# Performance work log

Hardware: AMD Instinct MI355X
Metric: run time of the kernel (lower is better)

## Reference

```python
import jax, jax.numpy as jnp
import numpy as np

N, L, D, H = 2, 2048, 1024, 16
Dh = D // H          # 64
HIST = 2048          # history_len
SCALE = D ** 0.5     # note: module scales by sqrt(model_dim), not sqrt(head_dim)


def setup_inputs() -> dict:
    key = jax.random.key(0)
    ks = jax.random.split(key, 10)
    f = lambda k, s, sc=1.0: jax.random.normal(k, s, dtype=jnp.float32) * sc
    i = jnp.arange(L)
    causal = i[None, :] > i[:, None]            # mask future
    old = i[None, :] <= i[:, None] - HIST       # mask beyond history window
    mask = causal | old                          # True = masked, (L, L)
    return {
        "values": f(ks[0], (N, L, D)),
        "keys": f(ks[1], (N, L, D)),
        "query": f(ks[2], (N, L, D)),
        "origin_values": f(ks[3], (N, L, D)),
        "origin_keys": f(ks[4], (N, L, D)),
        "Wv": f(ks[5], (Dh, Dh), 0.1),
        "Wk": f(ks[6], (Dh, Dh), 0.1),
        "Wq": f(ks[7], (Dh, Dh), 0.1),
        "fc_w": f(ks[8], (D, D), 0.03),
        "fc_b": jnp.zeros((D,), dtype=jnp.float32),
        "mask": mask,
    }


def reference(values, keys, query, origin_values, origin_keys, Wv, Wk, Wq, fc_w, fc_b, mask):
    # forward(..., ref_sample=True): mfpca_attention path.
    # origin_keys/values are projected exactly as the prior ref_sample=False call stored them.
    split = lambda x: x.reshape(N, L, H, Dh)
    v = split(values) @ Wv.T        # (N, L, H, Dh)  torch Linear: x @ W^T, no bias
    k = split(keys) @ Wk.T
    q = split(query) @ Wq.T
    ov = split(origin_values) @ Wv.T
    ok = split(origin_keys) @ Wk.T

    energy = jnp.einsum('nqhd,nkhd->nhqk', q, ok)       # (N, H, L, L)
    samp_energy = jnp.einsum('nlhd,nlhd->nhl', q, k)    # (N, H, L)
    eye = jnp.eye(L, dtype=bool)
    # energy.diagonal().copy_(samp_energy)
    energy = jnp.where(eye, samp_energy[:, :, None, :], energy)
    energy = jnp.where(mask, jnp.float32(-1e20), energy)
    scores = jax.nn.softmax(energy / SCALE, axis=-1)
    diag_scores = jnp.diagonal(scores, axis1=2, axis2=3)    # (N, H, L)
    scores_nodiag = jnp.where(eye, 0.0, scores)
    # NOTE: original einsum output is indexed by l (not q) -- reproduced faithfully.
    origin_attention = jnp.einsum('nhql,nlhd->nlhd', scores_nodiag, ov)
    samp_attention = jnp.einsum('nhl,nlhd->nlhd', diag_scores, v)
    attention = (samp_attention + origin_attention).reshape(N, L, D)
    return attention @ fc_w.T + fc_b
```

## Files before the change

### kernel.cpp

```cpp
#include <hip/hip_runtime.h>

#define NB 2
#define LL 2048
#define DD 1024
#define HH 16
#define NHH (NB*HH)
#define LT (LL/64)
#define KT16 (LL/16)
#define CEXP 0.0450842200277801f

typedef __bf16 bf16x8 __attribute__((ext_vector_type(8)));
typedef unsigned short u16x8 __attribute__((ext_vector_type(8)));
typedef float f32x4 __attribute__((ext_vector_type(4)));

#define MFMA16 __builtin_amdgcn_mfma_f32_16x16x32_bf16
#define EXP2 __builtin_amdgcn_exp2f

__device__ __forceinline__ unsigned short f2bf(float f) {
    unsigned u = __float_as_uint(f);
    return (unsigned short)((u + 0x7fffu + ((u >> 16) & 1u)) >> 16);
}
__device__ __forceinline__ float bf2f(unsigned short u) {
    return __uint_as_float(((unsigned)u) << 16);
}
__device__ __forceinline__ bf16x8 ldfrag(const unsigned short* p) {
    return *reinterpret_cast<const bf16x8*>(p);
}
__device__ __forceinline__ bf16x8 cvt8v(float4 a, float4 b) {
    u16x8 u;
    u[0]=f2bf(a.x); u[1]=f2bf(a.y); u[2]=f2bf(a.z); u[3]=f2bf(a.w);
    u[4]=f2bf(b.x); u[5]=f2bf(b.y); u[6]=f2bf(b.z); u[7]=f2bf(b.w);
    return __builtin_bit_cast(bf16x8, u);
}
__device__ __forceinline__ ushort4 pack4(f32x4 d, float sc) {
    ushort4 o;
    o.x = f2bf(d[0]*sc); o.y = f2bf(d[1]*sc); o.z = f2bf(d[2]*sc); o.w = f2bf(d[3]*sc);
    return o;
}
__device__ __forceinline__ void gload16(const unsigned short* g, unsigned short* l) {
    __builtin_amdgcn_global_load_lds(
        (const __attribute__((address_space(1))) unsigned int*)g,
        (__attribute__((address_space(3))) unsigned int*)l, 16, 0, 0);
}

__global__ __launch_bounds__(256) void prep_kernel(
    const float* __restrict__ Wk, const float* __restrict__ Wq,
    const float* __restrict__ Wv, unsigned short* __restrict__ wfrag,
    const float* __restrict__ fc_w, unsigned short* __restrict__ fcwb)
{
    const int bid = blockIdx.x;
    const int t = threadIdx.x;
    if (bid < 6) {
        const int s = bid * 256 + t;
        const int m = s >> 9;
        const int rem = s & 511;
        const int f = rem >> 6;
        const int lane = rem & 63;
        const int n16 = lane & 15, quad = lane >> 4;
        const int mt = f >> 1, half = f & 1;
        const float* W = (m == 0) ? Wk : (m == 1) ? Wq : Wv;
        const float* p = W + (mt*16 + n16)*64 + quad*8 + half*32;
        float4 a = *reinterpret_cast<const float4*>(p);
        float4 b = *reinterpret_cast<const float4*>(p + 4);
        *reinterpret_cast<bf16x8*>(wfrag + (size_t)s * 8) = cvt8v(a, b);
    } else {
        const int idx = (bid - 6) * 1024 + t * 4;
        float4 wv = *reinterpret_cast<const float4*>(fc_w + idx);
        ushort4 o;
        o.x = f2bf(wv.x); o.y = f2bf(wv.y); o.z = f2bf(wv.z); o.w = f2bf(wv.w);
        *reinterpret_cast<ushort4*>(fcwb + idx) = o;
    }
}

__global__ __launch_bounds__(256) void proj_kernel(
    const float* __restrict__ values, const float* __restrict__ keys,
    const float* __restrict__ query,  const float* __restrict__ ovals,
    const float* __restrict__ okeys,  const unsigned short* __restrict__ wfrag,
    unsigned short* __restrict__ qb, unsigned short* __restrict__ okb,
    unsigned short* __restrict__ vb, unsigned short* __restrict__ ovb,
    float* __restrict__ ediag)
{
    const int t = threadIdx.x;
    const int w = t >> 6;
    const int lane = t & 63;
    const int n16 = lane & 15;
    const int quad = lane >> 4;
    const int h = blockIdx.y;
    const int row = blockIdx.x * 64 + w * 16 + n16;
    const int nn = row >> 11;
    const int ll = row & 2047;
    const size_t xoff  = (size_t)row * DD + h * 64 + quad * 8;
    const size_t qbase = (((size_t)(nn * HH + h)) * LL + ll) * 64;
    const size_t vbase = (size_t)row * DD + h * 64;

    if (blockIdx.z == 0) {
        const float4* kp = reinterpret_cast<const float4*>(keys  + xoff);
        const float4* qp = reinterpret_cast<const float4*>(query + xoff);
        const float4* op = reinterpret_cast<const float4*>(okeys + xoff);
        float4 k0 = kp[0], k1 = kp[1], k2 = kp[8], k3 = kp[9];
        float4 q0 = qp[0], q1 = qp[1], q2 = qp[8], q3 = qp[9];
        float4 o0 = op[0], o1 = op[1], o2 = op[8], o3 = op[9];
        bf16x8 wk[8], wq[8];
#pragma unroll
        for (int f = 0; f < 8; ++f) {
            wk[f] = ldfrag(wfrag + (size_t)(f * 64 + lane) * 8);
            wq[f] = ldfrag(wfrag + (size_t)((8 + f) * 64 + lane) * 8);
        }
        bf16x8 xk0 = cvt8v(k0, k1), xk1 = cvt8v(k2, k3);
        bf16x8 xq0 = cvt8v(q0, q1), xq1 = cvt8v(q2, q3);
        bf16x8 xo0 = cvt8v(o0, o1), xo1 = cvt8v(o2, o3);
        f32x4 ka[4], qa[4];
#pragma unroll
        for (int mt = 0; mt < 4; ++mt) {
            f32x4 d = {0.f,0.f,0.f,0.f};
            d = MFMA16(wk[mt*2], xk0, d, 0,0,0);
            ka[mt] = MFMA16(wk[mt*2+1], xk1, d, 0,0,0);
        }
#pragma unroll
        for (int mt = 0; mt < 4; ++mt) {
            f32x4 d = {0.f,0.f,0.f,0.f};
            d = MFMA16(wq[mt*2], xq0, d, 0,0,0);
            qa[mt] = MFMA16(wq[mt*2+1], xq1, d, 0,0,0);
            *reinterpret_cast<ushort4*>(qb + qbase + mt*16 + quad*4) = pack4(qa[mt], CEXP);
        }
#pragma unroll
        for (int mt = 0; mt < 4; ++mt) {
            f32x4 d = {0.f,0.f,0.f,0.f};
            d = MFMA16(wk[mt*2], xo0, d, 0,0,0);
            d = MFMA16(wk[mt*2+1], xo1, d, 0,0,0);
            *reinterpret_cast<ushort4*>(okb + qbase + mt*16 + quad*4) = pack4(d, 1.0f);
        }
        float p = 0.f;
#pragma unroll
        for (int mt = 0; mt < 4; ++mt)
            p += qa[mt][0]*ka[mt][0] + qa[mt][1]*ka[mt][1]
               + qa[mt][2]*ka[mt][2] + qa[mt][3]*ka[mt][3];
        p += __shfl_xor(p, 16);
        p += __shfl_xor(p, 32);
        if (lane < 16)
            ediag[((size_t)(nn * HH + h)) * LL + ll] = p;
    } else {
        const float4* vp = reinterpret_cast<const float4*>(values + xoff);
        const float4* op = reinterpret_cast<const float4*>(ovals  + xoff);
        float4 v0 = vp[0], v1 = vp[1], v2 = vp[8], v3 = vp[9];
        float4 o0 = op[0], o1 = op[1], o2 = op[8], o3 = op[9];
        bf16x8 wv[8];
#pragma unroll
        for (int f = 0; f < 8; ++f)
            wv[f] = ldfrag(wfrag + (size_t)((16 + f) * 64 + lane) * 8);
        bf16x8 xv0 = cvt8v(v0, v1), xv1 = cvt8v(v2, v3);
        bf16x8 xo0 = cvt8v(o0, o1), xo1 = cvt8v(o2, o3);
#pragma unroll
        for (int mt = 0; mt < 4; ++mt) {
            f32x4 d = {0.f,0.f,0.f,0.f};
            d = MFMA16(wv[mt*2], xv0, d, 0,0,0);
            d = MFMA16(wv[mt*2+1], xv1, d, 0,0,0);
            *reinterpret_cast<ushort4*>(vb + vbase + mt*16 + quad*4) = pack4(d, 1.0f);
        }
#pragma unroll
        for (int mt = 0; mt < 4; ++mt) {
            f32x4 d = {0.f,0.f,0.f,0.f};
            d = MFMA16(wv[mt*2], xo0, d, 0,0,0);
            d = MFMA16(wv[mt*2+1], xo1, d, 0,0,0);
            *reinterpret_cast<ushort4*>(ovb + vbase + mt*16 + quad*4) = pack4(d, 1.0f);
        }
    }
}

__global__ __launch_bounds__(256) void zrow_part(
    const unsigned short* __restrict__ qb, const unsigned short* __restrict__ okb,
    float* __restrict__ Zbuf)
{
    __shared__ unsigned short slds[2][64 * 64];

    const int bid = blockIdx.x;
    const int nh = bid & 31;
    const int qt = 31 - (bid >> 5);
    const int t = threadIdx.x;
    const int w = t >> 6;
    const int lane = t & 63;
    const int n = lane & 15;
    const int quad = lane >> 4;
    const size_t base = (size_t)nh * (LL * 64);
    const size_t nhL = (size_t)nh * LL;

    const unsigned short* bp = qb + base + (size_t)(qt*64 + w*16 + n) * 64 + quad * 8;
    const bf16x8 bq0 = ldfrag(bp);
    const bf16x8 bq1 = ldfrag(bp + 32);

    const int srow = t >> 3;
    const int schunk = (t & 7) ^ (srow & 7);
    const int soff = srow * 64 + schunk * 8;
    const int nst = qt + 1;

    {
        const unsigned short* s0 = okb + base + soff;
        gload16(s0, &slds[0][t * 8]);
        gload16(s0 + 32 * 64, &slds[0][2048 + t * 8]);
    }
    __syncthreads();

    const int rs0 = (quad ^ (n & 7)) * 8;
    const int rs1 = ((quad + 4) ^ (n & 7)) * 8;

    float zacc = 0.f;
    int buf = 0;
    for (int si = 0; si < nst; ++si) {
        if (si + 1 < nst) {
            const unsigned short* s0 = okb + base + (size_t)((si + 1) * 64) * 64 + soff;
            gload16(s0, &slds[buf ^ 1][t * 8]);
            gload16(s0 + 32 * 64, &slds[buf ^ 1][2048 + t * 8]);
        }
        const unsigned short* S = &slds[buf][0];
        const bool dstrip = (si == qt);
#pragma unroll
        for (int sub = 0; sub < 4; ++sub) {
            if (dstrip && sub > w) continue;
            const int row = sub * 16 + n;
            const bf16x8 a0 = ldfrag(S + row * 64 + rs0);
            const bf16x8 a1 = ldfrag(S + row * 64 + rs1);
            f32x4 d = {0.f, 0.f, 0.f, 0.f};
            d = MFMA16(a0, bq0, d, 0, 0, 0);
            d = MFMA16(a1, bq1, d, 0, 0, 0);
            if (dstrip && sub == w) {
#pragma unroll
                for (int r = 0; r < 4; ++r)
                    if (quad * 4 + r < n) zacc += EXP2(d[r]);
            } else {
#pragma unroll
                for (int r = 0; r < 4; ++r) zacc += EXP2(d[r]);
            }
        }
        __syncthreads();
        buf ^= 1;
    }

    zacc += __shfl_down(zacc, 32);
    zacc += __shfl_down(zacc, 16);
    if (lane < 16)
        Zbuf[nhL + qt * 64 + w * 16 + lane] = zacc;
}

__global__ __launch_bounds__(256) void colsum_part(
    const unsigned short* __restrict__ qb, const unsigned short* __restrict__ okb,
    const float* __restrict__ Zbuf, const float* __restrict__ ediag,
    float* __restrict__ colsum)
{
    __shared__ unsigned short slds[2][64 * 64];
    __shared__ __align__(16) float izlds[2][64];

    const int bid = blockIdx.x;
    const int nh = bid & 31;
    const int lt = bid >> 5;
    const int t = threadIdx.x;
    const int w = t >> 6;
    const int lane = t & 63;
    const int n = lane & 15;
    const int quad = lane >> 4;
    const size_t base = (size_t)nh * (LL * 64);
    const size_t nhL = (size_t)nh * LL;

    const unsigned short* bp = okb + base + (size_t)(lt*64 + w*16 + n) * 64 + quad * 8;
    const bf16x8 bl0 = ldfrag(bp);
    const bf16x8 bl1 = ldfrag(bp + 32);

    const int srow = t >> 3;
    const int schunk = (t & 7) ^ (srow & 7);
    const int soff = srow * 64 + schunk * 8;
    const int nst = 32 - lt;
    const int q00 = lt * 64;

    {
        const unsigned short* s0 = qb + base + (size_t)q00 * 64 + soff;
        gload16(s0, &slds[0][t * 8]);
        gload16(s0 + 32 * 64, &slds[0][2048 + t * 8]);
        if (t < 64) {
            const float z = Zbuf[nhL + q00 + t];
            const float e = ediag[nhL + q00 + t];
            izlds[0][t] = 1.f / (z + EXP2(e * CEXP));
        }
    }
    __syncthreads();

    const int rs0 = (quad ^ (n & 7)) * 8;
    const int rs1 = ((quad + 4) ^ (n & 7)) * 8;

    float cacc = 0.f;
    int buf = 0;
    for (int si = 0; si < nst; ++si) {
        if (si + 1 < nst) {
            const int qn = q00 + (si + 1) * 64;
            const unsigned short* s0 = qb + base + (size_t)qn * 64 + soff;
            gload16(s0, &slds[buf ^ 1][t * 8]);
            gload16(s0 + 32 * 64, &slds[buf ^ 1][2048 + t * 8]);
            if (t < 64) {
                const float z = Zbuf[nhL + qn + t];
                const float e = ediag[nhL + qn + t];
                izlds[buf ^ 1][t] = 1.f / (z + EXP2(e * CEXP));
            }
        }
        const unsigned short* S = &slds[buf][0];
        const bool dstrip = (si == 0);
#pragma unroll
        for (int sub = 0; sub < 4; ++sub) {
            if (dstrip && sub < w) continue;
            const int row = sub * 16 + n;
            const bf16x8 a0 = ldfrag(S + row * 64 + rs0);
            const bf16x8 a1 = ldfrag(S + row * 64 + rs1);
            const f32x4 izv = *reinterpret_cast<const f32x4*>(&izlds[buf][sub * 16 + quad * 4]);
            f32x4 d = {0.f, 0.f, 0.f, 0.f};
            d = MFMA16(a0, bl0, d, 0, 0, 0);
            d = MFMA16(a1, bl1, d, 0, 0, 0);
            if (dstrip && sub == w) {
#pragma unroll
                for (int r = 0; r < 4; ++r)
                    if (quad * 4 + r > n) cacc += EXP2(d[r]) * izv[r];
            } else {
#pragma unroll
                for (int r = 0; r < 4; ++r) cacc += EXP2(d[r]) * izv[r];
            }
        }
        __syncthreads();
        buf ^= 1;
    }

    cacc += __shfl_down(cacc, 32);
    cacc += __shfl_down(cacc, 16);
    if (lane < 16)
        colsum[nhL + lt * 64 + w * 16 + lane] = cacc;
}

#define LOADA(vS, ovS, zS, eS, csS, k) do {                                \
    vS  = ldfrag(pv  + (k)*32);                                            \
    ovS = ldfrag(pov + (k)*32);                                            \
    zS  = Zbuf  [scbase + ((k)>>1)*LL];                                    \
    eS  = ediag [scbase + ((k)>>1)*LL];                                    \
    csS = colsum[scbase + ((k)>>1)*LL];                                    \
} while (0)

#define CVTWRITE(vS, ovS, zS, eS, csS, dst) do {                           \
    const float de_ = EXP2(eS * CEXP);                                     \
    const float ds_ = de_ * (1.f / (zS + de_));                            \
    u16x8 vu_ = __builtin_bit_cast(u16x8, vS);                             \
    u16x8 ou_ = __builtin_bit_cast(u16x8, ovS);                            \
    u16x8 o_;                                                              \
    _Pragma("unroll")                                                      \
    for (int i_ = 0; i_ < 8; ++i_)                                         \
        o_[i_] = f2bf(ds_ * bf2f(vu_[i_]) + csS * bf2f(ou_[i_]));          \
    *reinterpret_cast<u16x8*>(dst) = o_;                                   \
} while (0)

#define COMPUTE(Abuf, Bbuf) do {                                           \
    bf16x8 af_[4], bf_[2];                                                 \
    _Pragma("unroll")                                                      \
    for (int mt = 0; mt < 4; ++mt)                                         \
        af_[mt] = ldfrag((Abuf) + (wr*64 + mt*16 + n)*32 + quad*8);        \
    _Pragma("unroll")                                                      \
    for (int nt = 0; nt < 2; ++nt)                                         \
        bf_[nt] = ldfrag((Bbuf) + (wc*32 + nt*16 + n)*32 + quad*8);        \
    _Pragma("unroll")                                                      \
    for (int mt = 0; mt < 4; ++mt)                                         \
        _Pragma("unroll")                                                  \
        for (int nt = 0; nt < 2; ++nt)                                     \
            acc[mt][nt] = MFMA16(af_[mt], bf_[nt], acc[mt][nt], 0,0,0);    \
} while (0)

__global__ __launch_bounds__(512) void out_kernel(
    const unsigned short* __restrict__ vb, const unsigned short* __restrict__ ovb,
    const float* __restrict__ Zbuf, const float* __restrict__ ediag,
    const float* __restrict__ colsum,
    const unsigned short* __restrict__ fcwb, const float* __restrict__ fc_b,
    float* __restrict__ out)
{
    __shared__ unsigned short lds[2][2][128 * 32];

    const int bid = blockIdx.x;
    const int swz = (bid & 7) * 32 + (bid >> 3);
    const int ct = swz & 7;
    const int rt = swz >> 3;
    const int row0 = rt * 128, col0 = ct * 128;

    const int t = threadIdx.x;
    const int w = t >> 6, lane = t & 63;
    const int n = lane & 15, quad = lane >> 4;
    const int wr = w >> 2, wc = w & 3;

    const int arow = row0 + (t >> 2);
    const unsigned short* pv  = vb  + (size_t)arow * DD + (t & 3) * 8;
    const unsigned short* pov = ovb + (size_t)arow * DD + (t & 3) * 8;
    const int scbase = (arow >> 11) * (HH * LL) + (arow & 2047);
    const unsigned short* gb = fcwb + (size_t)(col0 + (t >> 2)) * DD + (t & 3) * 8;
    unsigned short* la0 = &lds[0][0][t * 8];
    unsigned short* lb0 = &lds[0][1][t * 8];
    unsigned short* la1 = &lds[1][0][t * 8];
    unsigned short* lb1 = &lds[1][1][t * 8];
    const unsigned short* A0 = &lds[0][0][0];
    const unsigned short* B0 = &lds[0][1][0];
    const unsigned short* A1 = &lds[1][0][0];
    const unsigned short* B1 = &lds[1][1][0];

    f32x4 acc[4][2];
#pragma unroll
    for (int mt = 0; mt < 4; ++mt)
#pragma unroll
        for (int nt = 0; nt < 2; ++nt) acc[mt][nt] = (f32x4){0.f, 0.f, 0.f, 0.f};

    bf16x8 vP, ovP, vQ, ovQ; float zP, eP, csP, zQ, eQ, csQ;
    LOADA(vP, ovP, zP, eP, csP, 0);
    LOADA(vQ, ovQ, zQ, eQ, csQ, 1);
    gload16(gb, lb0);
    CVTWRITE(vP, ovP, zP, eP, csP, la0);
    __syncthreads();

    for (int kt = 0; kt < 32; kt += 2) {
        gload16(gb + (kt + 1) * 32, lb1);
        if (kt + 2 < 32) LOADA(vP, ovP, zP, eP, csP, kt + 2);
        COMPUTE(A0, B0);
        CVTWRITE(vQ, ovQ, zQ, eQ, csQ, la1);
        __syncthreads();
        if (kt + 2 < 32) {
            gload16(gb + (kt + 2) * 32, lb0);
            if (kt + 3 < 32) LOADA(vQ, ovQ, zQ, eQ, csQ, kt + 3);
        }
        COMPUTE(A1, B1);
        if (kt + 2 < 32) CVTWRITE(vP, ovP, zP, eP, csP, la0);
        __syncthreads();
    }

#pragma unroll
    for (int nt = 0; nt < 2; ++nt) {
        const int col = col0 + wc * 32 + nt * 16 + n;
        const float bias = fc_b[col];
#pragma unroll
        for (int mt = 0; mt < 4; ++mt)
#pragma unroll
            for (int r = 0; r < 4; ++r)
                out[(size_t)(row0 + wr * 64 + mt * 16 + quad * 4 + r) * DD + col]
                    = acc[mt][nt][r] + bias;
    }
}

extern "C" void kernel_launch(void* const* d_in, const int* in_sizes, int n_in,
                              void* d_out, int out_size, void* d_ws, size_t ws_size,
                              hipStream_t stream) {
    const float* values = (const float*)d_in[0];
    const float* keys   = (const float*)d_in[1];
    const float* query  = (const float*)d_in[2];
    const float* ovals  = (const float*)d_in[3];
    const float* okeys  = (const float*)d_in[4];
    const float* Wv     = (const float*)d_in[5];
    const float* Wk     = (const float*)d_in[6];
    const float* Wq     = (const float*)d_in[7];
    const float* fc_w   = (const float*)d_in[8];
    const float* fc_b   = (const float*)d_in[9];
    float* out = (float*)d_out;

    float* ws      = (float*)d_ws;
    float* ediag   = ws;
    float* Zbuf    = ediag + 65536;
    float* colsum  = Zbuf + 65536;
    unsigned short* qb   = (unsigned short*)(colsum + 65536);
    unsigned short* okb  = qb   + 4194304;
    unsigned short* vb   = okb  + 4194304;
    unsigned short* ovb  = vb   + 4194304;
    unsigned short* fcwb = ovb  + 4194304;
    unsigned short* wfrag = fcwb + 1048576;

    prep_kernel<<<dim3(1030), 256, 0, stream>>>(Wk, Wq, Wv, wfrag, fc_w, fcwb);
    proj_kernel<<<dim3(64, 16, 2), 256, 0, stream>>>(
        values, keys, query, ovals, okeys, wfrag, qb, okb, vb, ovb, ediag);
    zrow_part<<<dim3(1024), 256, 0, stream>>>(qb, okb, Zbuf);
    colsum_part<<<dim3(1024), 256, 0, stream>>>(qb, okb, Zbuf, ediag, colsum);
    out_kernel<<<dim3(256), 512, 0, stream>>>(vb, ovb, Zbuf, ediag, colsum, fcwb, fc_b, out);
}
```

Measured before the change: 222.6 us.

## Process two query/key tiles per block and fold normalizer into MFMA accumulator

zrow_part and colsum_part now handle two 64-row tiles per block, so each LDS-staged strip feeds two sets of MFMAs and grid size halves. colsum replaces the per-element multiply by 1/Z with a -log2(Z) value preloaded into the MFMA accumulator, so the normalization happens inside exp2. The fc_w bf16 conversion moves from prep_kernel into an extra z-slice of proj_kernel, leaving prep_kernel with 6 blocks. This halves LDS reload traffic but reduces the number of blocks, adds register pressure, and gives tiles in the same block unequal amounts of triangular work.

Result: slower. 236.4 us (+6.2%).

```diff
diff --git a/kernel.cpp b/kernel.cpp
--- a/kernel.cpp
+++ b/kernel.cpp
@@ -15,6 +15,7 @@
 
 #define MFMA16 __builtin_amdgcn_mfma_f32_16x16x32_bf16
 #define EXP2 __builtin_amdgcn_exp2f
+#define LOG2 __builtin_amdgcn_logf
 
 __device__ __forceinline__ unsigned short f2bf(float f) {
     unsigned u = __float_as_uint(f);
@@ -45,42 +46,42 @@
 
 __global__ __launch_bounds__(256) void prep_kernel(
     const float* __restrict__ Wk, const float* __restrict__ Wq,
-    const float* __restrict__ Wv, unsigned short* __restrict__ wfrag,
-    const float* __restrict__ fc_w, unsigned short* __restrict__ fcwb)
+    const float* __restrict__ Wv, unsigned short* __restrict__ wfrag)
 {
-    const int bid = blockIdx.x;
     const int t = threadIdx.x;
-    if (bid < 6) {
-        const int s = bid * 256 + t;
-        const int m = s >> 9;
-        const int rem = s & 511;
-        const int f = rem >> 6;
-        const int lane = rem & 63;
-        const int n16 = lane & 15, quad = lane >> 4;
-        const int mt = f >> 1, half = f & 1;
-        const float* W = (m == 0) ? Wk : (m == 1) ? Wq : Wv;
-        const float* p = W + (mt*16 + n16)*64 + quad*8 + half*32;
-        float4 a = *reinterpret_cast<const float4*>(p);
-        float4 b = *reinterpret_cast<const float4*>(p + 4);
-        *reinterpret_cast<bf16x8*>(wfrag + (size_t)s * 8) = cvt8v(a, b);
-    } else {
-        const int idx = (bid - 6) * 1024 + t * 4;
-        float4 wv = *reinterpret_cast<const float4*>(fc_w + idx);
-        ushort4 o;
-        o.x = f2bf(wv.x); o.y = f2bf(wv.y); o.z = f2bf(wv.z); o.w = f2bf(wv.w);
-        *reinterpret_cast<ushort4*>(fcwb + idx) = o;
-    }
+    const int s = blockIdx.x * 256 + t;
+    const int m = s >> 9;
+    const int rem = s & 511;
+    const int f = rem >> 6;
+    const int lane = rem & 63;
+    const int n16 = lane & 15, quad = lane >> 4;
+    const int mt = f >> 1, half = f & 1;
+    const float* W = (m == 0) ? Wk : (m == 1) ? Wq : Wv;
+    const float* p = W + (mt*16 + n16)*64 + quad*8 + half*32;
+    float4 a = *reinterpret_cast<const float4*>(p);
+    float4 b = *reinterpret_cast<const float4*>(p + 4);
+    *reinterpret_cast<bf16x8*>(wfrag + (size_t)s * 8) = cvt8v(a, b);
 }
 
 __global__ __launch_bounds__(256) void proj_kernel(
     const float* __restrict__ values, const float* __restrict__ keys,
     const float* __restrict__ query,  const float* __restrict__ ovals,
     const float* __restrict__ okeys,  const unsigned short* __restrict__ wfrag,
+    const float* __restrict__ fc_w,   unsigned short* __restrict__ fcwb,
     unsigned short* __restrict__ qb, unsigned short* __restrict__ okb,
     unsigned short* __restrict__ vb, unsigned short* __restrict__ ovb,
     float* __restrict__ ediag)
 {
     const int t = threadIdx.x;
+    if (blockIdx.z == 2) {
+        const int id = blockIdx.y * 64 + blockIdx.x;
+        const int idx = id * 1024 + t * 4;
+        float4 wv = *reinterpret_cast<const float4*>(fc_w + idx);
+        ushort4 o;
+        o.x = f2bf(wv.x); o.y = f2bf(wv.y); o.z = f2bf(wv.z); o.w = f2bf(wv.w);
+        *reinterpret_cast<ushort4*>(fcwb + idx) = o;
+        return;
+    }
     const int w = t >> 6;
     const int lane = t & 63;
     const int n16 = lane & 15;
@@ -175,7 +176,7 @@
 
     const int bid = blockIdx.x;
     const int nh = bid & 31;
-    const int qt = 31 - (bid >> 5);
+    const int qt2 = 15 - (bid >> 5);
     const int t = threadIdx.x;
     const int w = t >> 6;
     const int lane = t & 63;
@@ -184,14 +185,18 @@
     const size_t base = (size_t)nh * (LL * 64);
     const size_t nhL = (size_t)nh * LL;
 
-    const unsigned short* bp = qb + base + (size_t)(qt*64 + w*16 + n) * 64 + quad * 8;
-    const bf16x8 bq0 = ldfrag(bp);
-    const bf16x8 bq1 = ldfrag(bp + 32);
+    bf16x8 bq[2][2];
+#pragma unroll
+    for (int h = 0; h < 2; ++h) {
+        const unsigned short* bp = qb + base
+            + (size_t)(qt2*128 + h*64 + w*16 + n) * 64 + quad * 8;
+        bq[h][0] = ldfrag(bp); bq[h][1] = ldfrag(bp + 32);
+    }
 
     const int srow = t >> 3;
     const int schunk = (t & 7) ^ (srow & 7);
     const int soff = srow * 64 + schunk * 8;
-    const int nst = qt + 1;
+    const int nst = 2 * qt2 + 2;
 
     {
         const unsigned short* s0 = okb + base + soff;
@@ -203,7 +208,7 @@
     const int rs0 = (quad ^ (n & 7)) * 8;
     const int rs1 = ((quad + 4) ^ (n & 7)) * 8;
 
-    float zacc = 0.f;
+    float zacc[2] = {0.f, 0.f};
     int buf = 0;
     for (int si = 0; si < nst; ++si) {
         if (si + 1 < nst) {
@@ -212,33 +217,42 @@
             gload16(s0 + 32 * 64, &slds[buf ^ 1][2048 + t * 8]);
         }
         const unsigned short* S = &slds[buf][0];
-        const bool dstrip = (si == qt);
 #pragma unroll
         for (int sub = 0; sub < 4; ++sub) {
-            if (dstrip && sub > w) continue;
             const int row = sub * 16 + n;
             const bf16x8 a0 = ldfrag(S + row * 64 + rs0);
             const bf16x8 a1 = ldfrag(S + row * 64 + rs1);
-            f32x4 d = {0.f, 0.f, 0.f, 0.f};
-            d = MFMA16(a0, bq0, d, 0, 0, 0);
-            d = MFMA16(a1, bq1, d, 0, 0, 0);
-            if (dstrip && sub == w) {
-#pragma unroll
-                for (int r = 0; r < 4; ++r)
-                    if (quad * 4 + r < n) zacc += EXP2(d[r]);
-            } else {
-#pragma unroll
-                for (int r = 0; r < 4; ++r) zacc += EXP2(d[r]);
+#pragma unroll
+            for (int h = 0; h < 2; ++h) {
+                const int qt_h = 2 * qt2 + h;
+                if (si > qt_h) continue;
+                const bool dstrip = (si == qt_h);
+                if (dstrip && sub > w) continue;
+                f32x4 d = {0.f, 0.f, 0.f, 0.f};
+                d = MFMA16(a0, bq[h][0], d, 0, 0, 0);
+                d = MFMA16(a1, bq[h][1], d, 0, 0, 0);
+                if (dstrip && sub == w) {
+#pragma unroll
+                    for (int r = 0; r < 4; ++r)
+                        if (quad * 4 + r < n) zacc[h] += EXP2(d[r]);
+                } else {
+#pragma unroll
+                    for (int r = 0; r < 4; ++r) zacc[h] += EXP2(d[r]);
+                }
             }
         }
         __syncthreads();
         buf ^= 1;
     }
 
-    zacc += __shfl_down(zacc, 32);
-    zacc += __shfl_down(zacc, 16);
-    if (lane < 16)
-        Zbuf[nhL + qt * 64 + w * 16 + lane] = zacc;
+#pragma unroll
+    for (int h = 0; h < 2; ++h) {
+        float z = zacc[h];
+        z += __shfl_down(z, 32);
+        z += __shfl_down(z, 16);
+        if (lane < 16)
+            Zbuf[nhL + qt2 * 128 + h * 64 + w * 16 + lane] = z;
+    }
 }
 
 __global__ __launch_bounds__(256) void colsum_part(
@@ -251,7 +265,7 @@
 
     const int bid = blockIdx.x;
     const int nh = bid & 31;
-    const int lt = bid >> 5;
+    const int lt2 = bid >> 5;
     const int t = threadIdx.x;
     const int w = t >> 6;
     const int lane = t & 63;
@@ -260,15 +274,19 @@
     const size_t base = (size_t)nh * (LL * 64);
     const size_t nhL = (size_t)nh * LL;
 
-    const unsigned short* bp = okb + base + (size_t)(lt*64 + w*16 + n) * 64 + quad * 8;
-    const bf16x8 bl0 = ldfrag(bp);
-    const bf16x8 bl1 = ldfrag(bp + 32);
+    bf16x8 bl[2][2];
+#pragma unroll
+    for (int h = 0; h < 2; ++h) {
+        const unsigned short* bp = okb + base
+            + (size_t)(lt2*128 + h*64 + w*16 + n) * 64 + quad * 8;
+        bl[h][0] = ldfrag(bp); bl[h][1] = ldfrag(bp + 32);
+    }
 
     const int srow = t >> 3;
     const int schunk = (t & 7) ^ (srow & 7);
     const int soff = srow * 64 + schunk * 8;
-    const int nst = 32 - lt;
-    const int q00 = lt * 64;
+    const int nst = 32 - 2 * lt2;
+    const int q00 = lt2 * 128;
 
     {
         const unsigned short* s0 = qb + base + (size_t)q00 * 64 + soff;
@@ -277,7 +295,7 @@
         if (t < 64) {
             const float z = Zbuf[nhL + q00 + t];
             const float e = ediag[nhL + q00 + t];
-            izlds[0][t] = 1.f / (z + EXP2(e * CEXP));
+            izlds[0][t] = -LOG2(z + EXP2(e * CEXP));
         }
     }
     __syncthreads();
@@ -285,7 +303,7 @@
     const int rs0 = (quad ^ (n & 7)) * 8;
     const int rs1 = ((quad + 4) ^ (n & 7)) * 8;
 
-    float cacc = 0.f;
+    float cacc[2] = {0.f, 0.f};
     int buf = 0;
     for (int si = 0; si < nst; ++si) {
         if (si + 1 < nst) {
@@ -296,38 +314,47 @@
             if (t < 64) {
                 const float z = Zbuf[nhL + qn + t];
                 const float e = ediag[nhL + qn + t];
-                izlds[buf ^ 1][t] = 1.f / (z + EXP2(e * CEXP));
+                izlds[buf ^ 1][t] = -LOG2(z + EXP2(e * CEXP));
             }
         }
         const unsigned short* S = &slds[buf][0];
-        const bool dstrip = (si == 0);
 #pragma unroll
         for (int sub = 0; sub < 4; ++sub) {
-            if (dstrip && sub < w) continue;
             const int row = sub * 16 + n;
             const bf16x8 a0 = ldfrag(S + row * 64 + rs0);
             const bf16x8 a1 = ldfrag(S + row * 64 + rs1);
-            const f32x4 izv = *reinterpret_cast<const f32x4*>(&izlds[buf][sub * 16 + quad * 4]);
-            f32x4 d = {0.f, 0.f, 0.f, 0.f};
-            d = MFMA16(a0, bl0, d, 0, 0, 0);
-            d = MFMA16(a1, bl1, d, 0, 0, 0);
-            if (dstrip && sub == w) {
-#pragma unroll
-                for (int r = 0; r < 4; ++r)
-                    if (quad * 4 + r > n) cacc += EXP2(d[r]) * izv[r];
-            } else {
-#pragma unroll
-                for (int r = 0; r < 4; ++r) cacc += EXP2(d[r]) * izv[r];
+            const f32x4 lgv = *reinterpret_cast<const f32x4*>(
+                &izlds[buf][sub * 16 + quad * 4]);
+#pragma unroll
+            for (int h = 0; h < 2; ++h) {
+                if (si < h) continue;
+                const bool dstrip = (si == h);
+                if (dstrip && sub < w) continue;
+                f32x4 d = lgv;
+                d = MFMA16(a0, bl[h][0], d, 0, 0, 0);
+                d = MFMA16(a1, bl[h][1], d, 0, 0, 0);
+                if (dstrip && sub == w) {
+#pragma unroll
+                    for (int r = 0; r < 4; ++r)
+                        if (quad * 4 + r > n) cacc[h] += EXP2(d[r]);
+                } else {
+#pragma unroll
+                    for (int r = 0; r < 4; ++r) cacc[h] += EXP2(d[r]);
+                }
             }
         }
         __syncthreads();
         buf ^= 1;
     }
 
-    cacc += __shfl_down(cacc, 32);
-    cacc += __shfl_down(cacc, 16);
-    if (lane < 16)
-        colsum[nhL + lt * 64 + w * 16 + lane] = cacc;
+#pragma unroll
+    for (int h = 0; h < 2; ++h) {
+        float c = cacc[h];
+        c += __shfl_down(c, 32);
+        c += __shfl_down(c, 16);
+        if (lane < 16)
+            colsum[nhL + lt2 * 128 + h * 64 + w * 16 + lane] = c;
+    }
 }
 
 #define LOADA(vS, ovS, zS, eS, csS, k) do {                                \
@@ -466,10 +493,11 @@
     unsigned short* fcwb = ovb  + 4194304;
     unsigned short* wfrag = fcwb + 1048576;
 
-    prep_kernel<<<dim3(1030), 256, 0, stream>>>(Wk, Wq, Wv, wfrag, fc_w, fcwb);
-    proj_kernel<<<dim3(64, 16, 2), 256, 0, stream>>>(
-        values, keys, query, ovals, okeys, wfrag, qb, okb, vb, ovb, ediag);
-    zrow_part<<<dim3(1024), 256, 0, stream>>>(qb, okb, Zbuf);
-    colsum_part<<<dim3(1024), 256, 0, stream>>>(qb, okb, Zbuf, ediag, colsum);
+    prep_kernel<<<dim3(6), 256, 0, stream>>>(Wk, Wq, Wv, wfrag);
+    proj_kernel<<<dim3(64, 16, 3), 256, 0, stream>>>(
+        values, keys, query, ovals, okeys, wfrag, fc_w, fcwb,
+        qb, okb, vb, ovb, ediag);
+    zrow_part<<<dim3(512), 256, 0, stream>>>(qb, okb, Zbuf);
+    colsum_part<<<dim3(512), 256, 0, stream>>>(qb, okb, Zbuf, ediag, colsum);
     out_kernel<<<dim3(256), 512, 0, stream>>>(vb, ovb, Zbuf, ediag, colsum, fcwb, fc_b, out);
 }
```
